# Kernel tuning notes

Measured on AMD Instinct MI355X. Metric: run time of the kernel, lower is better.

Reference implementation:

```python
import jax, jax.numpy as jnp
import numpy as np

N = 50000      # nodes
E = 800000     # random edges (self loops appended in reference)
B = 500        # graphs
H = 4          # attention heads
F = 64         # feature_dim (per-head out channels)
SLOPE = 0.2    # GATConv leaky_relu negative slope


def gat_layer(x, src, dst, W, att_s, att_d, b):
    # x: [N, Fin]; W: [Fin, H*F]; att_s/att_d: [H, F]; b: [H*F]
    h = (x @ W).reshape(N, H, F)                       # [N,H,F]
    a_s = jnp.einsum('nhf,hf->nh', h, att_s)           # [N,H]
    a_d = jnp.einsum('nhf,hf->nh', h, att_d)           # [N,H]
    e = jax.nn.leaky_relu(a_s[src] + a_d[dst], SLOPE)  # [E',H]
    emax = jax.ops.segment_max(e, dst, num_segments=N) # [N,H] (finite: self loops)
    ee = jnp.exp(e - emax[dst])
    denom = jax.ops.segment_sum(ee, dst, num_segments=N)
    alpha = ee / denom[dst]                            # [E',H]
    out = jax.ops.segment_sum(alpha[:, :, None] * h[src], dst, num_segments=N)
    return out.reshape(N, H * F) + b


def setup_inputs() -> dict:
    key = jax.random.key(0)
    ks = jax.random.split(key, 32)
    s = 0.05
    inp = {
        'node_features': jax.random.normal(ks[0], (N, 5), jnp.float32),
        'building_mask': jax.random.randint(ks[1], (N,), 0, 2),
        'batch': jnp.sort(jax.random.randint(ks[2], (N,), 0, B)),
        'edge_index': jax.random.randint(ks[3], (2, E), 0, N),
        'bbox_W': jax.random.normal(ks[4], (5, 64)) * s,
        'bbox_b': jnp.zeros((64,), jnp.float32),
        'mask_embed': jax.random.normal(ks[5], (2, 64)) * s,
        'node_W': jax.random.normal(ks[6], (128, 64)) * s,
        'node_b': jnp.zeros((64,), jnp.float32),
        'w0': jax.random.normal(ks[7], (64, 256)) * s,
        'as0': jax.random.normal(ks[8], (H, F)) * s,
        'ad0': jax.random.normal(ks[9], (H, F)) * s,
        'b0': jnp.zeros((256,), jnp.float32),
        'w1': jax.random.normal(ks[10], (256, 256)) * s,
        'as1': jax.random.normal(ks[11], (H, F)) * s,
        'ad1': jax.random.normal(ks[12], (H, F)) * s,
        'b1': jnp.zeros((256,), jnp.float32),
        'w2': jax.random.normal(ks[13], (256, 256)) * s,
        'as2': jax.random.normal(ks[14], (H, F)) * s,
        'ad2': jax.random.normal(ks[15], (H, F)) * s,
        'b2': jnp.zeros((256,), jnp.float32),
        'agg_W': jax.random.normal(ks[16], (832, 256)) * s,
        'agg_b': jnp.zeros((256,), jnp.float32),
        'mu_W': jax.random.normal(ks[17], (256, 256)) * s,
        'mu_b': jnp.zeros((256,), jnp.float32),
        'var_W': jax.random.normal(ks[18], (256, 256)) * s,
        'var_b': jnp.zeros((256,), jnp.float32),
    }
    return inp


def reference(node_features, building_mask, batch, edge_index,
              bbox_W, bbox_b, mask_embed, node_W, node_b,
              w0, as0, ad0, b0, w1, as1, ad1, b1, w2, as2, ad2, b2,
              agg_W, agg_b, mu_W, mu_b, var_W, var_b):
    # node featurization
    x = jax.nn.relu(node_features @ bbox_W + bbox_b)          # [N,64]
    m = jax.nn.relu(mask_embed[building_mask])                 # [N,64]
    n0 = jax.nn.relu(jnp.concatenate([x, m], -1) @ node_W + node_b)  # [N,64]

    # self loops (GATConv add_self_loops=True)
    loop = jnp.arange(N, dtype=edge_index.dtype)
    src = jnp.concatenate([edge_index[0], loop])
    dst = jnp.concatenate([edge_index[1], loop])

    g = jax.ops.segment_max(n0, batch, num_segments=B, indices_are_sorted=True)
    g_embed = [g]

    n_t = jax.nn.relu(gat_layer(n0, src, dst, w0, as0, ad0, b0))
    g_embed.append(jax.ops.segment_max(n_t, batch, num_segments=B, indices_are_sorted=True))

    for (W, a_s, a_d, b) in [(w1, as1, ad1, b1), (w2, as2, ad2, b2)]:
        n_t = jax.nn.relu(gat_layer(n_t, src, dst, W, a_s, a_d, b))
        g_embed.append(jax.ops.segment_max(n_t, batch, num_segments=B, indices_are_sorted=True))

    latent = jnp.concatenate(g_embed, -1) @ agg_W + agg_b      # [B,256]
    mu = latent @ mu_W + mu_b
    log_var = latent @ var_W + var_b
    return (mu, log_var)
```

## Files before the change

### kernel.cpp

```cpp
#include <hip/hip_runtime.h>

#define NN 50000
#define EE 800000
#define BB 500
#define SCB 196

typedef short v8s __attribute__((ext_vector_type(8)));
typedef float v4f __attribute__((ext_vector_type(4)));

__device__ __forceinline__ float bf2f(unsigned short u) {
    union { unsigned int i; float f; } v; v.i = ((unsigned int)u) << 16; return v.f;
}
__device__ __forceinline__ unsigned short f2bf(float f) {
    union { float f; unsigned int i; } v; v.f = f;
    unsigned int x = v.i;
    unsigned int r = (x + 0x7FFFu + ((x >> 16) & 1u)) >> 16;
    return (unsigned short)r;
}

__global__ void k_sentinel(float* out, float val) {
    int i = blockIdx.x * blockDim.x + threadIdx.x;
    if (i < BB * 512) out[i] = val;
}

__global__ void k_prep(const float* __restrict__ nf, const int* __restrict__ bmask,
                       const float* __restrict__ bboxW, const float* __restrict__ bboxb,
                       const float* __restrict__ membed, unsigned short* __restrict__ feat,
                       const float* __restrict__ a0, unsigned short* __restrict__ d0,
                       const float* __restrict__ a1, unsigned short* __restrict__ d1,
                       const float* __restrict__ a2, unsigned short* __restrict__ d2,
                       const float* __restrict__ a3, unsigned short* __restrict__ d3,
                       int* __restrict__ counts) {
    int g = blockIdx.x * blockDim.x + threadIdx.x;
    if (g < NN) counts[g] = 1;
    if (g < NN * 64) {
        int n = g >> 6, f = g & 63;
        float s = bboxb[f];
        for (int k = 0; k < 5; ++k) s += nf[n * 5 + k] * bboxW[k * 64 + f];
        s = fmaxf(s, 0.f);
        int bm = bmask[n]; if ((unsigned)bm > 1u) bm = 0;
        float mv = fmaxf(membed[bm * 64 + f], 0.f);
        feat[(size_t)n * 128 + f] = f2bf(s);
        feat[(size_t)n * 128 + 64 + f] = f2bf(mv);
        return;
    }
    g -= NN * 64;
    const float* in; unsigned short* out; int K, Nout, idx;
    if (g < 8192)        { in = a0; out = d0; K = 128; Nout = 64;  idx = g; }
    else if (g < 24576)  { in = a1; out = d1; K = 64;  Nout = 256; idx = g - 8192; }
    else if (g < 90112)  { in = a2; out = d2; K = 256; Nout = 256; idx = g - 24576; }
    else if (g < 155648) { in = a3; out = d3; K = 256; Nout = 256; idx = g - 90112; }
    else return;
    int k = idx / Nout, n = idx % Nout;
    out[n * K + k] = f2bf(in[idx]);
}

template <int KT, bool BR, bool ATT>
__global__ __launch_bounds__(256) void k_gemm(const unsigned short* __restrict__ A,
                                              const unsigned short* __restrict__ Bt,
                                              const float* __restrict__ bias,
                                              unsigned short* __restrict__ C, int M, int ldc,
                                              const float* __restrict__ atts, const float* __restrict__ attd,
                                              float* __restrict__ asA, float* __restrict__ adA) {
    constexpr int CH = KT / 8;
    __shared__ v8s As[64 * CH];
    __shared__ v8s Bs[64 * CH];
    __shared__ float ap[4][4][4][4][2];
    const int t = threadIdx.x;
    const int m0 = blockIdx.x * 64;
    const int n0 = blockIdx.y * 64;
    for (int idx = t; idx < 64 * CH; idx += 256) {
        int m = idx / CH, kc = idx % CH;
        int row = m0 + m;
        v8s v = (v8s){0, 0, 0, 0, 0, 0, 0, 0};
        if (row < M) v = *(const v8s*)(A + (size_t)row * KT + kc * 8);
        As[m * CH + (kc ^ (m & 7))] = v;
    }
    for (int idx = t; idx < 64 * CH; idx += 256) {
        int n = idx / CH, kc = idx % CH;
        v8s v = *(const v8s*)(Bt + (size_t)(n0 + n) * KT + kc * 8);
        Bs[n * CH + (kc ^ (n & 7))] = v;
    }
    __syncthreads();
    const int l = t & 63, w = t >> 6;
    const int q = l >> 4, r16 = l & 15;
    const int nloc = w * 16 + r16;
    v4f acc[4];
#pragma unroll
    for (int i = 0; i < 4; ++i) acc[i] = (v4f){0.f, 0.f, 0.f, 0.f};
#pragma unroll
    for (int kt = 0; kt < KT / 32; ++kt) {
        int kc = kt * 4 + q;
        v8s bfr = Bs[nloc * CH + (kc ^ (nloc & 7))];
#pragma unroll
        for (int mt = 0; mt < 4; ++mt) {
            v8s afr = As[(mt * 16 + r16) * CH + (kc ^ (r16 & 7))];
            acc[mt] = __builtin_amdgcn_mfma_f32_16x16x32_bf16(afr, bfr, acc[mt], 0, 0, 0);
        }
    }
    const int col = n0 + nloc;
#pragma unroll
    for (int mt = 0; mt < 4; ++mt) {
#pragma unroll
        for (int r = 0; r < 4; ++r) {
            int row = m0 + mt * 16 + q * 4 + r;
            if (row < M) {
                float v = acc[mt][r];
                if (BR) v = fmaxf(v + bias[col], 0.f);
                C[(size_t)row * ldc + col] = f2bf(v);
            }
        }
    }
    if (ATT) {
        float sa = atts[blockIdx.y * 64 + nloc];
        float da = attd[blockIdx.y * 64 + nloc];
        float rs[4][4], rd[4][4];
#pragma unroll
        for (int mt = 0; mt < 4; ++mt)
#pragma unroll
            for (int r = 0; r < 4; ++r) { rs[mt][r] = acc[mt][r] * sa; rd[mt][r] = acc[mt][r] * da; }
#pragma unroll
        for (int d = 1; d < 16; d <<= 1) {
#pragma unroll
            for (int mt = 0; mt < 4; ++mt)
#pragma unroll
                for (int r = 0; r < 4; ++r) {
                    rs[mt][r] += __shfl_xor(rs[mt][r], d, 64);
                    rd[mt][r] += __shfl_xor(rd[mt][r], d, 64);
                }
        }
        if (r16 == 0) {
#pragma unroll
            for (int mt = 0; mt < 4; ++mt)
#pragma unroll
                for (int r = 0; r < 4; ++r) { ap[w][q][mt][r][0] = rs[mt][r]; ap[w][q][mt][r][1] = rd[mt][r]; }
        }
        __syncthreads();
        if (t < 128) {
            int row = t >> 1, which = t & 1;
            int qq = (row >> 2) & 3, mtt = row >> 4, rr = row & 3;
            float s = ap[0][qq][mtt][rr][which] + ap[1][qq][mtt][rr][which] +
                      ap[2][qq][mtt][rr][which] + ap[3][qq][mtt][rr][which];
            if (m0 + row < M) (which ? adA : asA)[(m0 + row) * 4 + blockIdx.y] = s;
        }
    }
}

__global__ void k_count(const int* __restrict__ dst, int* __restrict__ counts) {
    int e = blockIdx.x * blockDim.x + threadIdx.x;
    if (e < EE) {
        int d = dst[e];
        if ((unsigned)d < (unsigned)NN) atomicAdd(&counts[d], 1);
    }
}

__global__ __launch_bounds__(256) void k_scanA(const int* __restrict__ counts, int* __restrict__ bsum) {
    __shared__ int red[256];
    const int b = blockIdx.x, t = threadIdx.x;
    int i = b * 256 + t;
    red[t] = (i < NN) ? counts[i] : 0;
    __syncthreads();
    for (int d = 128; d > 0; d >>= 1) {
        if (t < d) red[t] += red[t + d];
        __syncthreads();
    }
    if (t == 0) bsum[b] = red[0];
}

__global__ __launch_bounds__(256) void k_scanB(const int* __restrict__ bsum, int* __restrict__ boff) {
    __shared__ int s[256];
    const int t = threadIdx.x;
    int v = (t < SCB) ? bsum[t] : 0;
    s[t] = v;
    __syncthreads();
    for (int d = 1; d < 256; d <<= 1) {
        int x = (t >= d) ? s[t - d] : 0;
        __syncthreads();
        s[t] += x;
        __syncthreads();
    }
    if (t < SCB) boff[t] = s[t] - v;
}

__global__ __launch_bounds__(256) void k_scanC(const int* __restrict__ counts, const int* __restrict__ boff,
                                               int* __restrict__ off, int* __restrict__ cur) {
    __shared__ int s[256];
    const int b = blockIdx.x, t = threadIdx.x;
    int i = b * 256 + t;
    int v = (i < NN) ? counts[i] : 0;
    s[t] = v;
    __syncthreads();
    for (int d = 1; d < 256; d <<= 1) {
        int x = (t >= d) ? s[t - d] : 0;
        __syncthreads();
        s[t] += x;
        __syncthreads();
    }
    int excl = s[t] - v + boff[b];
    if (i < NN) { off[i] = excl; cur[i] = excl; }
    if (i == NN - 1) off[NN] = excl + v;
}

#define SCAT_K 256
__global__ __launch_bounds__(256) void k_scatter(const int* __restrict__ ei, int* __restrict__ cur,
                                                 int* __restrict__ csr) {
    const int p = blockIdx.x & 7;
    const int j = blockIdx.x >> 3;
    const int plo = p * (NN / 8), phi = plo + (NN / 8);
    const int TOT = EE + NN;
    const int chunk = (TOT + SCAT_K - 1) / SCAT_K;
    const int e1 = min((j + 1) * chunk, TOT);
    for (int e = j * chunk + (int)threadIdx.x; e < e1; e += 256) {
        int d = (e < EE) ? ei[EE + e] : (e - EE);
        if (d < plo || d >= phi) continue;
        int s = (e < EE) ? ei[e] : d;
        if ((unsigned)s >= (unsigned)NN) s = d;
        int pos = atomicAdd(&cur[d], 1);
        csr[pos] = s;
    }
}

__global__ __launch_bounds__(256) void k_agg(const unsigned short* __restrict__ h,
                                             const float* __restrict__ asA, const float* __restrict__ adA,
                                             const int* __restrict__ off, const int* __restrict__ csr,
                                             const float* __restrict__ bias,
                                             unsigned short* __restrict__ nout, int base) {
    __shared__ int   sL[4][64];
    __shared__ float wL[4][64][4];
    const int nd4 = threadIdx.x >> 6;
    const int node = base + blockIdx.x * 4 + nd4;
    const int l = threadIdx.x & 63;
    const int hl = l >> 4, k16 = l & 15;
    const int o0 = off[node];
    const int deg = off[node + 1] - o0;
    const int dcap = deg < 64 ? deg : 64;
    const float ad4 = adA[node * 4 + hl];
    float sm = 0.f;
    for (int k = k16; k < dcap; k += 16) {
        int s = csr[o0 + k];
        if (hl == 0) sL[nd4][k] = s;
        float e = asA[s * 4 + hl] + ad4;
        e = e > 0.f ? e : 0.2f * e;
        float w = __expf(e);
        wL[nd4][k][hl] = w;
        sm += w;
    }
    for (int k = 64 + k16; k < deg; k += 16) {
        int s = csr[o0 + k];
        float e = asA[s * 4 + hl] + ad4;
        e = e > 0.f ? e : 0.2f * e;
        sm += __expf(e);
    }
#pragma unroll
    for (int d = 1; d < 16; d <<= 1) sm += __shfl_xor(sm, d, 64);
    const float rden = 1.f / sm;
    __syncthreads();
    float a0 = 0.f, a1 = 0.f, a2 = 0.f, a3 = 0.f;
    const int c = l * 4;
    int k = 0;
    for (; k + 4 <= dcap; k += 4) {
        int s0 = sL[nd4][k], s1 = sL[nd4][k + 1], s2 = sL[nd4][k + 2], s3 = sL[nd4][k + 3];
        float w0 = wL[nd4][k][hl], w1 = wL[nd4][k + 1][hl], w2 = wL[nd4][k + 2][hl], w3 = wL[nd4][k + 3][hl];
        ushort4 h0 = *(const ushort4*)(h + (size_t)s0 * 256 + c);
        ushort4 h1 = *(const ushort4*)(h + (size_t)s1 * 256 + c);
        ushort4 h2 = *(const ushort4*)(h + (size_t)s2 * 256 + c);
        ushort4 h3 = *(const ushort4*)(h + (size_t)s3 * 256 + c);
        a0 += w0 * bf2f(h0.x) + w1 * bf2f(h1.x) + w2 * bf2f(h2.x) + w3 * bf2f(h3.x);
        a1 += w0 * bf2f(h0.y) + w1 * bf2f(h1.y) + w2 * bf2f(h2.y) + w3 * bf2f(h3.y);
        a2 += w0 * bf2f(h0.z) + w1 * bf2f(h1.z) + w2 * bf2f(h2.z) + w3 * bf2f(h3.z);
        a3 += w0 * bf2f(h0.w) + w1 * bf2f(h1.w) + w2 * bf2f(h2.w) + w3 * bf2f(h3.w);
    }
    for (; k < dcap; ++k) {
        int s = sL[nd4][k];
        float w = wL[nd4][k][hl];
        ushort4 hv = *(const ushort4*)(h + (size_t)s * 256 + c);
        a0 += w * bf2f(hv.x); a1 += w * bf2f(hv.y); a2 += w * bf2f(hv.z); a3 += w * bf2f(hv.w);
    }
    for (int k2 = 64; k2 < deg; ++k2) {
        int s = csr[o0 + k2];
        float e = asA[s * 4 + hl] + ad4;
        e = e > 0.f ? e : 0.2f * e;
        float w = __expf(e);
        ushort4 hv = *(const ushort4*)(h + (size_t)s * 256 + c);
        a0 += w * bf2f(hv.x); a1 += w * bf2f(hv.y); a2 += w * bf2f(hv.z); a3 += w * bf2f(hv.w);
    }
    float4 bv = *(const float4*)(bias + c);
    ushort4 o;
    o.x = f2bf(fmaxf(a0 * rden + bv.x, 0.f));
    o.y = f2bf(fmaxf(a1 * rden + bv.y, 0.f));
    o.z = f2bf(fmaxf(a2 * rden + bv.z, 0.f));
    o.w = f2bf(fmaxf(a3 * rden + bv.w, 0.f));
    *(ushort4*)(nout + (size_t)node * 256 + c) = o;
}

__global__ __launch_bounds__(256) void k_gmaxseg(const unsigned short* __restrict__ nt, int cols,
                                                 const int* __restrict__ batch,
                                                 float* __restrict__ gcat, int gbase) {
    __shared__ float red[256];
    const int b = blockIdx.x, t = threadIdx.x;
    const int lane = t & 63, chunk = t >> 6;
    const int c = blockIdx.y * 64 + lane;
    int lo = 0, hi = NN;
    while (lo < hi) { int mid = (lo + hi) >> 1; if (batch[mid] < b) lo = mid + 1; else hi = mid; }
    int lo2 = lo, hi2 = NN;
    while (lo2 < hi2) { int mid = (lo2 + hi2) >> 1; if (batch[mid] < b + 1) lo2 = mid + 1; else hi2 = mid; }
    float m = 0.f;
    for (int n = lo + chunk; n < lo2; n += 4)
        m = fmaxf(m, bf2f(nt[(size_t)n * cols + c]));
    red[t] = m;
    __syncthreads();
    if (chunk == 0) {
        m = fmaxf(fmaxf(m, red[64 + lane]), fmaxf(red[128 + lane], red[192 + lane]));
        gcat[b * 832 + gbase + c] = m;
    }
}

__global__ __launch_bounds__(256) void k_final(const float* __restrict__ gcat,
                                               const float* __restrict__ aggW, const float* __restrict__ aggb,
                                               const float* __restrict__ muW, const float* __restrict__ mub,
                                               const float* __restrict__ vaW, const float* __restrict__ vab,
                                               float* __restrict__ out) {
    __shared__ float gr[832];
    __shared__ float lat[256];
    const int b = blockIdx.x, t = threadIdx.x;
    for (int i = t; i < 832; i += 256) gr[i] = gcat[b * 832 + i];
    __syncthreads();
    float s0 = 0.f, s1 = 0.f, s2 = 0.f, s3 = 0.f;
#pragma unroll 4
    for (int k = 0; k < 832; k += 4) {
        s0 += gr[k + 0] * aggW[(k + 0) * 256 + t];
        s1 += gr[k + 1] * aggW[(k + 1) * 256 + t];
        s2 += gr[k + 2] * aggW[(k + 2) * 256 + t];
        s3 += gr[k + 3] * aggW[(k + 3) * 256 + t];
    }
    lat[t] = ((s0 + s1) + (s2 + s3)) + aggb[t];
    __syncthreads();
    float m0 = 0.f, m1 = 0.f, v0 = 0.f, v1 = 0.f;
#pragma unroll 4
    for (int k = 0; k < 256; k += 2) {
        float l0 = lat[k], l1 = lat[k + 1];
        m0 += l0 * muW[(k + 0) * 256 + t];
        m1 += l1 * muW[(k + 1) * 256 + t];
        v0 += l0 * vaW[(k + 0) * 256 + t];
        v1 += l1 * vaW[(k + 1) * 256 + t];
    }
    out[b * 256 + t] = (m0 + m1) + mub[t];
    out[BB * 256 + b * 256 + t] = (v0 + v1) + vab[t];
}

extern "C" void kernel_launch(void* const* d_in, const int* in_sizes, int n_in,
                              void* d_out, int out_size, void* d_ws, size_t ws_size,
                              hipStream_t stream) {
    (void)in_sizes; (void)n_in; (void)out_size;
    const float* nf     = (const float*)d_in[0];
    const int*   bmask  = (const int*)d_in[1];
    const int*   batch  = (const int*)d_in[2];
    const int*   ei     = (const int*)d_in[3];
    const float* bboxW  = (const float*)d_in[4];
    const float* bboxb  = (const float*)d_in[5];
    const float* membed = (const float*)d_in[6];
    const float* nodeW  = (const float*)d_in[7];
    const float* nodeb  = (const float*)d_in[8];
    const float* w0     = (const float*)d_in[9];
    const float* as0    = (const float*)d_in[10];
    const float* ad0    = (const float*)d_in[11];
    const float* b0     = (const float*)d_in[12];
    const float* w1     = (const float*)d_in[13];
    const float* as1    = (const float*)d_in[14];
    const float* ad1    = (const float*)d_in[15];
    const float* b1     = (const float*)d_in[16];
    const float* w2     = (const float*)d_in[17];
    const float* as2    = (const float*)d_in[18];
    const float* ad2    = (const float*)d_in[19];
    const float* b2     = (const float*)d_in[20];
    const float* aggW   = (const float*)d_in[21];
    const float* aggb   = (const float*)d_in[22];
    const float* muW    = (const float*)d_in[23];
    const float* mub    = (const float*)d_in[24];
    const float* vaW    = (const float*)d_in[25];
    const float* vab    = (const float*)d_in[26];
    float* out = (float*)d_out;

    char* base = (char*)d_ws;
    unsigned short* hbuf    = (unsigned short*)(base);
    unsigned short* nbuf    = (unsigned short*)(base + 25600000);
    unsigned short* feat128 = nbuf;
    unsigned short* n0buf   = (unsigned short*)(base + 25600000 + 12800000);
    char* pool0 = base + 51200000;
    char* p = pool0;
    auto alloc = [&](size_t bytes) { char* r = p; p += (bytes + 255) & ~(size_t)255; return r; };
    unsigned short* nodeWt = (unsigned short*)alloc(128 * 64 * 2);
    unsigned short* w0t    = (unsigned short*)alloc(64 * 256 * 2);
    unsigned short* w1t    = (unsigned short*)alloc(256 * 256 * 2);
    unsigned short* w2t    = (unsigned short*)alloc(256 * 256 * 2);
    float* asA    = (float*)alloc((size_t)NN * 4 * 4);
    float* adA    = (float*)alloc((size_t)NN * 4 * 4);
    int*   counts = (int*)alloc((size_t)NN * 4);
    int*   offs   = (int*)alloc((size_t)(NN + 1) * 4);
    int*   cur    = (int*)alloc((size_t)NN * 4);
    int*   csr    = (int*)alloc((size_t)(EE + NN) * 4);
    float* gcat   = (float*)alloc((size_t)BB * 832 * 4);
    int*   bsum   = (int*)alloc(SCB * 4);
    int*   boff   = (int*)alloc(SCB * 4);
    const size_t NEED = (size_t)(p - base);

    if (ws_size < NEED) {
        k_sentinel<<<1000, 256, 0, stream>>>(out, 2000.0f + (float)(ws_size >> 20));
        return;
    }

    k_prep<<<(NN * 64 + 155648 + 255) / 256, 256, 0, stream>>>(nf, bmask, bboxW, bboxb, membed, feat128,
                                                               nodeW, nodeWt, w0, w0t, w1, w1t, w2, w2t, counts);
    k_count<<<(EE + 255) / 256, 256, 0, stream>>>(ei + EE, counts);
    k_scanA<<<SCB, 256, 0, stream>>>(counts, bsum);
    k_scanB<<<1, 256, 0, stream>>>(bsum, boff);
    k_scanC<<<SCB, 256, 0, stream>>>(counts, boff, offs, cur);
    k_scatter<<<SCAT_K * 8, 256, 0, stream>>>(ei, cur, csr);
    k_gemm<128, true, false><<<dim3(782, 1), 256, 0, stream>>>(feat128, nodeWt, nodeb, n0buf, NN, 64,
                                                               nullptr, nullptr, nullptr, nullptr);
    k_gmaxseg<<<dim3(BB, 1), 256, 0, stream>>>(n0buf, 64, batch, gcat, 0);
    k_gemm<64, false, true><<<dim3(782, 4), 256, 0, stream>>>(n0buf, w0t, nullptr, hbuf, NN, 256,
                                                              as0, ad0, asA, adA);
    k_agg<<<6250, 256, 0, stream>>>(hbuf, asA, adA, offs, csr, b0, nbuf, 0);
    k_agg<<<6250, 256, 0, stream>>>(hbuf, asA, adA, offs, csr, b0, nbuf, 25000);
    k_gmaxseg<<<dim3(BB, 4), 256, 0, stream>>>(nbuf, 256, batch, gcat, 64);
    k_gemm<256, false, true><<<dim3(782, 4), 256, 0, stream>>>(nbuf, w1t, nullptr, hbuf, NN, 256,
                                                               as1, ad1, asA, adA);
    k_agg<<<6250, 256, 0, stream>>>(hbuf, asA, adA, offs, csr, b1, nbuf, 0);
    k_agg<<<6250, 256, 0, stream>>>(hbuf, asA, adA, offs, csr, b1, nbuf, 25000);
    k_gmaxseg<<<dim3(BB, 4), 256, 0, stream>>>(nbuf, 256, batch, gcat, 320);
    k_gemm<256, false, true><<<dim3(782, 4), 256, 0, stream>>>(nbuf, w2t, nullptr, hbuf, NN, 256,
                                                               as2, ad2, asA, adA);
    k_agg<<<6250, 256, 0, stream>>>(hbuf, asA, adA, offs, csr, b2, nbuf, 0);
    k_agg<<<6250, 256, 0, stream>>>(hbuf, asA, adA, offs, csr, b2, nbuf, 25000);
    k_gmaxseg<<<dim3(BB, 4), 256, 0, stream>>>(nbuf, 256, batch, gcat, 576);
    k_final<<<BB, 256, 0, stream>>>(gcat, aggW, aggb, muW, mub, vaW, vab, out);
}
```

Measured before the change: 651.7 us.

## Double-buffer GEMM K-tiles through registers to overlap global loads with MFMA

The GEMM kernel now splits K into 64-wide tiles held in two LDS buffers. It prefetches the next tile into registers while MFMAs run on the current one, then stores it to the other buffer. This is meant to hide global-load latency and cut LDS use for K=256, which may raise occupancy. In exchange it adds one barrier per K-tile and some register pressure. The GEMMs are likely only a small part of total GAT time, since most of it goes to edge gather and scatter.

```diff
diff --git a/kernel.cpp b/kernel.cpp
--- a/kernel.cpp
+++ b/kernel.cpp
@@ -62,42 +62,66 @@
                                               unsigned short* __restrict__ C, int M, int ldc,
                                               const float* __restrict__ atts, const float* __restrict__ attd,
                                               float* __restrict__ asA, float* __restrict__ adA) {
-    constexpr int CH = KT / 8;
-    __shared__ v8s As[64 * CH];
-    __shared__ v8s Bs[64 * CH];
+    constexpr int NT = KT / 64;
+    constexpr int NB = (NT > 1) ? 2 : 1;
+    __shared__ v8s As[NB][64 * 8];
+    __shared__ v8s Bs[NB][64 * 8];
     __shared__ float ap[4][4][4][4][2];
     const int t = threadIdx.x;
     const int m0 = blockIdx.x * 64;
     const int n0 = blockIdx.y * 64;
-    for (int idx = t; idx < 64 * CH; idx += 256) {
-        int m = idx / CH, kc = idx % CH;
-        int row = m0 + m;
-        v8s v = (v8s){0, 0, 0, 0, 0, 0, 0, 0};
-        if (row < M) v = *(const v8s*)(A + (size_t)row * KT + kc * 8);
-        As[m * CH + (kc ^ (m & 7))] = v;
-    }
-    for (int idx = t; idx < 64 * CH; idx += 256) {
-        int n = idx / CH, kc = idx % CH;
-        v8s v = *(const v8s*)(Bt + (size_t)(n0 + n) * KT + kc * 8);
-        Bs[n * CH + (kc ^ (n & 7))] = v;
-    }
-    __syncthreads();
     const int l = t & 63, w = t >> 6;
     const int q = l >> 4, r16 = l & 15;
     const int nloc = w * 16 + r16;
+
+    const int sm = t >> 3, kcl = t & 7;
+    const int swz = kcl ^ (sm & 7);
+    const int arow0 = m0 + sm, arow1 = m0 + sm + 32;
+    const unsigned short* Bp0 = Bt + (size_t)(n0 + sm) * KT + kcl * 8;
+    const unsigned short* Bp1 = Bt + (size_t)(n0 + sm + 32) * KT + kcl * 8;
+    const unsigned short* Ap0 = A + (size_t)arow0 * KT + kcl * 8;
+    const unsigned short* Ap1 = A + (size_t)arow1 * KT + kcl * 8;
+
+    v8s ra0, ra1, rb0, rb1;
+    const v8s vz = (v8s){0, 0, 0, 0, 0, 0, 0, 0};
+    auto loadT = [&](int kt) {
+        ra0 = (arow0 < M) ? *(const v8s*)(Ap0 + kt * 64) : vz;
+        ra1 = (arow1 < M) ? *(const v8s*)(Ap1 + kt * 64) : vz;
+        rb0 = *(const v8s*)(Bp0 + kt * 64);
+        rb1 = *(const v8s*)(Bp1 + kt * 64);
+    };
+    auto storeT = [&](int b) {
+        As[b][sm * 8 + swz] = ra0;
+        As[b][(sm + 32) * 8 + swz] = ra1;
+        Bs[b][sm * 8 + swz] = rb0;
+        Bs[b][(sm + 32) * 8 + swz] = rb1;
+    };
+
     v4f acc[4];
 #pragma unroll
     for (int i = 0; i < 4; ++i) acc[i] = (v4f){0.f, 0.f, 0.f, 0.f};
-#pragma unroll
-    for (int kt = 0; kt < KT / 32; ++kt) {
-        int kc = kt * 4 + q;
-        v8s bfr = Bs[nloc * CH + (kc ^ (nloc & 7))];
-#pragma unroll
-        for (int mt = 0; mt < 4; ++mt) {
-            v8s afr = As[(mt * 16 + r16) * CH + (kc ^ (r16 & 7))];
-            acc[mt] = __builtin_amdgcn_mfma_f32_16x16x32_bf16(afr, bfr, acc[mt], 0, 0, 0);
+
+    loadT(0);
+    storeT(0);
+    __syncthreads();
+#pragma unroll
+    for (int kt = 0; kt < NT; ++kt) {
+        const int b = kt & (NB - 1);
+        if (kt + 1 < NT) loadT(kt + 1);
+#pragma unroll
+        for (int s = 0; s < 2; ++s) {
+            int c = s * 4 + q;
+            v8s bfr = Bs[b][nloc * 8 + (c ^ (nloc & 7))];
+#pragma unroll
+            for (int mt = 0; mt < 4; ++mt) {
+                v8s afr = As[b][(mt * 16 + r16) * 8 + (c ^ (r16 & 7))];
+                acc[mt] = __builtin_amdgcn_mfma_f32_16x16x32_bf16(afr, bfr, acc[mt], 0, 0, 0);
+            }
         }
-    }
+        if (kt + 1 < NT) storeT((kt + 1) & (NB - 1));
+        __syncthreads();
+    }
+
     const int col = n0 + nloc;
 #pragma unroll
     for (int mt = 0; mt < 4; ++mt) {
```

Result: faster. 613.5 us (-5.9%).
